# Performance work log

Hardware: AMD Instinct MI355X
Metric: run time of the kernel (lower is better)

Reference implementation:

```python
import jax, jax.numpy as jnp
import numpy as np

KUP = 5       # reassembly kernel size
DELTA = 2     # upsample ratio
KENC = 3      # encoder conv kernel size
CM = 64       # compressed channels
INC = 256
OUTC = 256


def conv2d(x, w, b, pad):
    # x: (N,C,H,W), w: (O,I,kh,kw)
    y = jax.lax.conv_general_dilated(
        x, w, window_strides=(1, 1), padding=[(pad, pad), (pad, pad)],
        dimension_numbers=("NCHW", "OIHW", "NCHW"))
    return y + b[None, :, None, None]


def pixel_shuffle(x, r):
    # torch semantics: channel c*r^2 + i*r + j -> (c, h*r+i, w*r+j)
    N, Cr2, H, W = x.shape
    C = Cr2 // (r * r)
    x = x.reshape(N, C, r, r, H, W)
    x = x.transpose(0, 1, 4, 2, 5, 3)
    return x.reshape(N, C, H * r, W * r)


def setup_inputs() -> dict:
    key = jax.random.key(0)
    ks = jax.random.split(key, 7)
    N, H, W = 4, 64, 64
    x = jax.random.normal(ks[0], (N, INC, H, W), dtype=jnp.float32)
    w_down = jax.random.normal(ks[1], (CM, INC, 1, 1), dtype=jnp.float32) * 0.05
    b_down = jnp.zeros((CM,), jnp.float32)
    enc_out = DELTA * DELTA * KUP * KUP  # 100
    w_enc = jax.random.normal(ks[2], (enc_out, CM, KENC, KENC), dtype=jnp.float32) * 0.05
    b_enc = jnp.zeros((enc_out,), jnp.float32)
    w_out = jax.random.normal(ks[3], (OUTC, INC, 1, 1), dtype=jnp.float32) * 0.05
    b_out = jnp.zeros((OUTC,), jnp.float32)
    return {"in_tensor": x, "w_down": w_down, "b_down": b_down,
            "w_enc": w_enc, "b_enc": b_enc, "w_out": w_out, "b_out": b_out}


def reference(in_tensor, w_down, b_down, w_enc, b_enc, w_out, b_out):
    N, C, H, W = in_tensor.shape
    k2, d2 = KUP * KUP, DELTA * DELTA

    # --- kernel prediction branch ---
    k = conv2d(in_tensor, w_down, b_down, 0)          # (N, Cm, H, W)
    k = conv2d(k, w_enc, b_enc, KENC // 2)            # (N, k2*d2, H, W)
    # pixel_shuffle + per-upsampled-pixel softmax over Kup^2, fused:
    # channel index = kup_idx * delta^2 + subpixel_idx (torch pixel_shuffle layout)
    k = k.reshape(N, k2, d2, H, W)
    k = jax.nn.softmax(k, axis=1)
    kern = k.transpose(0, 3, 4, 1, 2)                 # (N, H, W, k2, d2)

    # --- feature reassembly ---
    pad = KUP // 2
    xp = jnp.pad(in_tensor, ((0, 0), (0, 0), (pad, pad), (pad, pad)))
    # (N, C, H, W, Kup^2); k index = kh*Kup + kw, matching torch unfold order
    patches = jnp.stack(
        [xp[:, :, i:i + H, j:j + W] for i in range(KUP) for j in range(KUP)],
        axis=-1)

    out = jnp.einsum("nchwk,nhwkd->nhwcd", patches, kern)  # (N,H,W,C,d2)
    out = out.reshape(N, H, W, C * d2).transpose(0, 3, 1, 2)  # (N, C*d2, H, W)
    out = pixel_shuffle(out, DELTA)                   # (N, C, H*delta, W*delta)

    return conv2d(out, w_out, b_out, 0)               # (N, outC, H*delta, W*delta)
```

## Files before the change

### kernel.cpp

```cpp
#include <hip/hip_runtime.h>
#include <hip/hip_bf16.h>


namespace {
constexpr int kN = 4, kH = 64, kW = 64, kINC = 256, kCM = 64;
constexpr int kENC = 100, kH2 = 128, kW2 = 128, kOUTC = 256;
constexpr int kHW = kH * kW;
constexpr int kHW2 = kH2 * kW2;
constexpr int kPadW = 66;
constexpr int kTImg = kPadW * kPadW * kCM;
constexpr int kZPad = 68;
constexpr int kZImg = kZPad * kZPad * kOUTC;
constexpr int kPrepRepackEnc = 9 * 7 * 2 * 512;
constexpr int kPrepRepackWoz = 8 * 20 * 512;
constexpr int kPrepHaloZ = 4 * 528 * 16;
constexpr int kPrepHaloD = 4 * 260 * 8;
constexpr int kPrepTotal = kPrepRepackEnc + kPrepRepackWoz + kPrepHaloZ + kPrepHaloD;
}

typedef __attribute__((ext_vector_type(8))) short short8;
typedef __attribute__((ext_vector_type(4))) float floatx4;

static __device__ __forceinline__ unsigned short bf16bits(float f) {
  __hip_bfloat16 h = __float2bfloat16(f);
  return *(unsigned short*)&h;
}

__global__ __launch_bounds__(256) void k_prep(
    const float* __restrict__ we, unsigned short* __restrict__ Aswz,
    const float* __restrict__ wd, const float* __restrict__ wo,
    unsigned short* __restrict__ Awoz,
    float* __restrict__ zT, __hip_bfloat16* __restrict__ downT) {
  const int t = blockIdx.x * 256 + threadIdx.x;
  if (t < kPrepRepackEnc) {
    const int e = t;
    const int j = e & 7, lane = (e >> 3) & 63, kh = (e >> 9) & 1, tm = e >> 10;
    const int mt = tm % 7, tap = tm / 7;
    const int o = mt * 16 + (lane & 15);
    const int ci = kh * 32 + ((lane >> 4) & 3) * 8 + j;
    const float v = (o < kENC) ? we[(size_t)o * 576 + ci * 9 + tap] : 0.f;
    Aswz[e] = bf16bits(v);
  } else if (t < kPrepRepackEnc + kPrepRepackWoz) {
    const int e = t - kPrepRepackEnc;
    const int j = e & 7, lane = (e >> 3) & 63;
    const int rest = e >> 9;
    const int mt = rest % 20, ks = rest / 20;
    const int r = mt * 16 + (lane & 15);
    const int k = ks * 32 + (lane >> 4) * 8 + j;
    const float v = (r < kCM) ? wd[(size_t)r * kINC + k]
                              : wo[(size_t)(r - kCM) * kINC + k];
    Awoz[e] = bf16bits(v);
  } else if (t < kPrepTotal) {
    const int u0 = t - (kPrepRepackEnc + kPrepRepackWoz);
    if (u0 < kPrepHaloZ) {
      const int chunk = u0 & 15, rest = u0 >> 4;
      const int i = rest % 528, n = rest / 528;
      int r, c;
      if (i < 272) { r = i / 68; if (r >= 2) r += 64; c = i % 68; }
      else { const int j = i - 272; r = 2 + (j >> 2); const int cc = j & 3; c = (cc < 2) ? cc : cc + 64; }
      float4* p = (float4*)(zT + (size_t)n * kZImg + ((size_t)r * kZPad + c) * kOUTC) + chunk;
      *p = make_float4(0.f, 0.f, 0.f, 0.f);
    } else {
      const int u = u0 - kPrepHaloZ;
      const int chunk = u & 7, rest = u >> 3;
      const int i = rest % 260, n = rest / 260;
      int r, c;
      if (i < 132) { r = (i / 66) ? 65 : 0; c = i % 66; }
      else { const int j = i - 132; r = 1 + (j >> 1); c = (j & 1) ? 65 : 0; }
      float4* p = (float4*)((char*)downT
                  + ((size_t)n * kTImg + ((size_t)r * kPadW + c) * kCM) * 2) + chunk;
      *p = make_float4(0.f, 0.f, 0.f, 0.f);
    }
  }
}

__global__ __launch_bounds__(256) void k_dzmfma(
    const float* __restrict__ x, const unsigned short* __restrict__ Awoz,
    const float* __restrict__ bd, __hip_bfloat16* __restrict__ downT,
    float* __restrict__ zT) {
  const int b = blockIdx.x;
  const int pt = b & 255, n = b >> 8;
  const int wave = threadIdx.x >> 6, lane = threadIdx.x & 63;
  const int col = lane & 15, quad = lane >> 4;
  const int px = pt * 16 + col;
  const int h = px >> 6, w = px & 63;
  const float* xb = x + (size_t)n * kINC * kHW + px;

  floatx4 acc[5];
#pragma unroll
  for (int m = 0; m < 5; ++m) acc[m] = (floatx4){0.f, 0.f, 0.f, 0.f};

#pragma unroll
  for (int ks = 0; ks < 8; ++ks) {
    float xv[8];
#pragma unroll
    for (int j = 0; j < 8; ++j)
      xv[j] = xb[(size_t)(ks * 32 + quad * 8 + j) * kHW];
    short8 bf;
#pragma unroll
    for (int j = 0; j < 8; ++j) bf[j] = (short)bf16bits(xv[j]);
#pragma unroll
    for (int m = 0; m < 5; ++m) {
      const int wtile = wave * 5 + m;
      const short8 af = *(const short8*)(
          Awoz + ((size_t)(ks * 20 + wtile) * 64 + lane) * 8);
      acc[m] = __builtin_amdgcn_mfma_f32_16x16x32_bf16(af, bf, acc[m], 0, 0, 0);
    }
  }

#pragma unroll
  for (int m = 0; m < 5; ++m) {
    const int wtile = wave * 5 + m;
    const int r0 = wtile * 16 + quad * 4;
    if (wtile < 4) {
      union { unsigned short u[4]; uint2 v; } pk;
#pragma unroll
      for (int rr = 0; rr < 4; ++rr)
        pk.u[rr] = bf16bits(acc[m][rr] + bd[r0 + rr]);
      __hip_bfloat16* dst = downT + (size_t)n * kTImg
                            + ((h + 1) * kPadW + (w + 1)) * kCM + r0;
      *(uint2*)dst = pk.v;
    } else {
      const int o = r0 - kCM;
      float* dst = zT + (size_t)n * kZImg
                   + ((h + 2) * kZPad + (w + 2)) * kOUTC + o;
      *(float4*)dst = make_float4(acc[m][0], acc[m][1], acc[m][2], acc[m][3]);
    }
  }
}

__global__ __launch_bounds__(256) void k_encmfma(
    const __hip_bfloat16* __restrict__ downT,
    const unsigned short* __restrict__ Aswz,
    const float* __restrict__ be, float* __restrict__ enc) {
  const int b = blockIdx.x;
  const int h = b & 63, mtp = (b >> 6) & 3, n = b >> 8;
  const int wave = threadIdx.x >> 6, lane = threadIdx.x & 63;
  const int w0 = wave << 4;
  const int col = lane & 15, quad = lane >> 4;
  const int mt0 = mtp * 2;
  const bool has2 = (mt0 + 1) < 7;
  const short* dT = (const short*)downT + (size_t)n * kTImg;
  floatx4 acc0 = {0.f, 0.f, 0.f, 0.f}, acc1 = {0.f, 0.f, 0.f, 0.f};
#pragma unroll
  for (int tap = 0; tap < 9; ++tap) {
    const int dh = tap / 3 - 1, dw = tap % 3 - 1;
    const int rowbase = ((h + 1 + dh) * kPadW + (w0 + col + 1 + dw)) * kCM
                        + quad * 8;
#pragma unroll
    for (int kh = 0; kh < 2; ++kh) {
      const short8 bf = *(const short8*)(dT + rowbase + kh * 32);
      const short8 a0 = *(const short8*)(
          Aswz + (((size_t)(tap * 7 + mt0) * 2 + kh) * 64 + lane) * 8);
      acc0 = __builtin_amdgcn_mfma_f32_16x16x32_bf16(a0, bf, acc0, 0, 0, 0);
      if (has2) {
        const short8 a1 = *(const short8*)(
            Aswz + (((size_t)(tap * 7 + mt0 + 1) * 2 + kh) * 64 + lane) * 8);
        acc1 = __builtin_amdgcn_mfma_f32_16x16x32_bf16(a1, bf, acc1, 0, 0, 0);
      }
    }
  }
  const int p = h * kW + w0 + col;
#pragma unroll
  for (int r = 0; r < 4; ++r) {
    const int o = mt0 * 16 + quad * 4 + r;
    if (o < kENC) enc[(size_t)(n * kENC + o) * kHW + p] = acc0[r] + be[o];
  }
  if (has2) {
#pragma unroll
    for (int r = 0; r < 4; ++r) {
      const int o = (mt0 + 1) * 16 + quad * 4 + r;
      if (o < kENC) enc[(size_t)(n * kENC + o) * kHW + p] = acc1[r] + be[o];
    }
  }
}

__global__ __launch_bounds__(256) void k_fused_out(
    const float* __restrict__ zT, const float* __restrict__ enc,
    const float* __restrict__ bo, float* __restrict__ out) {
  const int b = blockIdx.x;
  const int pt = b & 255, og = (b >> 8) & 3, n = b >> 10;
  const int tid = threadIdx.x;
  const int wave = tid >> 6, lane = tid & 63;
  const int h = pt >> 2, w0 = (pt & 3) << 4;
  const int px0 = pt * 16;

  __shared__ float lds[64 * 65];
  float* kernLDS = lds;

  {
    const int p = tid & 15, chb = tid >> 4;
#pragma unroll
    for (int r = 0; r < 7; ++r) {
      const int ch = r * 16 + chb;
      if (ch < kENC)
        kernLDS[p * 104 + ch] = enc[((size_t)n * kENC + ch) * kHW + px0 + p];
    }
  }
  __syncthreads();

  if (tid < 64) {
    const int p = tid >> 2, d = tid & 3;
    float* kb = kernLDS + p * 104 + d;
    float m = -1e30f;
#pragma unroll
    for (int k = 0; k < 25; ++k) m = fmaxf(m, kb[k * 4]);
    float s = 0.f;
#pragma unroll
    for (int k = 0; k < 25; ++k) {
      const float e = __expf(kb[k * 4] - m);
      kb[k * 4] = e;
      s += e;
    }
    const float inv = 1.f / s;
#pragma unroll
    for (int k = 0; k < 25; ++k) kb[k * 4] *= inv;
  }
  __syncthreads();

  const int oc = lane & 15, pxi = lane >> 4;
  const int px_l = wave * 4 + pxi;
  const int w = w0 + px_l;
  const int o_l = oc * 4;
  const float* zb = zT + (size_t)n * kZImg + og * 64 + o_l;
  const float* kp = kernLDS + px_l * 104;
  float acc[4][4] = {};
#pragma unroll
  for (int tap = 0; tap < 25; ++tap) {
    const int kh = tap / 5, kw = tap % 5;
    const float4 zf = *(const float4*)(
        zb + ((size_t)(h + kh) * kZPad + (w + kw)) * kOUTC);
    const float4 kf = *(const float4*)(kp + tap * 4);
    acc[0][0] += zf.x * kf.x; acc[0][1] += zf.x * kf.y; acc[0][2] += zf.x * kf.z; acc[0][3] += zf.x * kf.w;
    acc[1][0] += zf.y * kf.x; acc[1][1] += zf.y * kf.y; acc[1][2] += zf.y * kf.z; acc[1][3] += zf.y * kf.w;
    acc[2][0] += zf.z * kf.x; acc[2][1] += zf.z * kf.y; acc[2][2] += zf.z * kf.z; acc[2][3] += zf.z * kf.w;
    acc[3][0] += zf.w * kf.x; acc[3][1] += zf.w * kf.y; acc[3][2] += zf.w * kf.z; acc[3][3] += zf.w * kf.w;
  }

  __syncthreads();
#pragma unroll
  for (int oi = 0; oi < 4; ++oi)
#pragma unroll
    for (int d = 0; d < 4; ++d)
      lds[(o_l + oi) * 65 + px_l * 4 + d] = acc[oi][d];
  __syncthreads();

  const int ol2 = tid >> 2, q = tid & 3;
  const int o = og * 64 + ol2;
  const float bias = bo[o];
  const float* Trow = lds + ol2 * 65;
#pragma unroll
  for (int i = 0; i < 2; ++i) {
    float* row = out + ((size_t)(n * kOUTC + o) * kH2 + (2 * h + i)) * kW2 + 2 * w0;
#pragma unroll
    for (int s = 0; s < 2; ++s) {
      const int xb_ = s * 16 + q * 4;
      float4 v;
      v.x = Trow[((xb_ + 0) >> 1) * 4 + i * 2 + ((xb_ + 0) & 1)] + bias;
      v.y = Trow[((xb_ + 1) >> 1) * 4 + i * 2 + ((xb_ + 1) & 1)] + bias;
      v.z = Trow[((xb_ + 2) >> 1) * 4 + i * 2 + ((xb_ + 2) & 1)] + bias;
      v.w = Trow[((xb_ + 3) >> 1) * 4 + i * 2 + ((xb_ + 3) & 1)] + bias;
      *(float4*)(row + xb_) = v;
    }
  }
}

extern "C" void kernel_launch(void* const* d_in, const int* in_sizes, int n_in,
                              void* d_out, int out_size, void* d_ws, size_t ws_size,
                              hipStream_t stream) {
  const float* x  = (const float*)d_in[0];
  const float* wd = (const float*)d_in[1];
  const float* bd = (const float*)d_in[2];
  const float* we = (const float*)d_in[3];
  const float* be = (const float*)d_in[4];
  const float* wo = (const float*)d_in[5];
  const float* bo = (const float*)d_in[6];
  float* out = (float*)d_out;

  float* enc = (float*)d_ws;
  float* zT  = enc + 1638400;
  __hip_bfloat16* downT = (__hip_bfloat16*)(zT + 4734976);
  unsigned short* Aswz  = (unsigned short*)(downT + (size_t)kN * kTImg);
  unsigned short* Awoz  = Aswz + 64512;

  k_prep<<<737, 256, 0, stream>>>(we, Aswz, wd, wo, Awoz, zT, downT);
  k_dzmfma<<<1024, 256, 0, stream>>>(x, Awoz, bd, downT, zT);
  k_encmfma<<<1024, 256, 0, stream>>>(downT, Aswz, be, enc);
  k_fused_out<<<4096, 256, 0, stream>>>(zT, enc, bo, out);
}
```

Baseline: 146.0 us.

## Fuse encoder conv into reassembly kernel, computing kernel logits per tile in LDS

Drops the separate encoder MFMA kernel and its global enc buffer. Each reassembly block now loads a 3x18x64 bf16 halo slab of the compressed features into LDS, runs the 3x3 encoder conv with MFMA for its 16 pixels, and writes the logits straight into LDS for the softmax. This removes one launch and the write and reread of the enc tensor. In exchange, the encoder conv is recomputed four times, once per output-channel group block, and each block does more work before the reassembly loop.

Result: slower. 156.7 us (+7.3%).

```diff
diff --git a/kernel.cpp b/kernel.cpp
--- a/kernel.cpp
+++ b/kernel.cpp
@@ -11,6 +11,7 @@
 constexpr int kTImg = kPadW * kPadW * kCM;
 constexpr int kZPad = 68;
 constexpr int kZImg = kZPad * kZPad * kOUTC;
+constexpr int kKP = 108;
 constexpr int kPrepRepackEnc = 9 * 7 * 2 * 512;
 constexpr int kPrepRepackWoz = 8 * 20 * 512;
 constexpr int kPrepHaloZ = 4 * 528 * 16;
@@ -129,79 +130,76 @@
   }
 }
 
-__global__ __launch_bounds__(256) void k_encmfma(
-    const __hip_bfloat16* __restrict__ downT,
-    const unsigned short* __restrict__ Aswz,
-    const float* __restrict__ be, float* __restrict__ enc) {
-  const int b = blockIdx.x;
-  const int h = b & 63, mtp = (b >> 6) & 3, n = b >> 8;
-  const int wave = threadIdx.x >> 6, lane = threadIdx.x & 63;
-  const int w0 = wave << 4;
-  const int col = lane & 15, quad = lane >> 4;
-  const int mt0 = mtp * 2;
-  const bool has2 = (mt0 + 1) < 7;
-  const short* dT = (const short*)downT + (size_t)n * kTImg;
-  floatx4 acc0 = {0.f, 0.f, 0.f, 0.f}, acc1 = {0.f, 0.f, 0.f, 0.f};
-#pragma unroll
-  for (int tap = 0; tap < 9; ++tap) {
-    const int dh = tap / 3 - 1, dw = tap % 3 - 1;
-    const int rowbase = ((h + 1 + dh) * kPadW + (w0 + col + 1 + dw)) * kCM
-                        + quad * 8;
-#pragma unroll
-    for (int kh = 0; kh < 2; ++kh) {
-      const short8 bf = *(const short8*)(dT + rowbase + kh * 32);
-      const short8 a0 = *(const short8*)(
-          Aswz + (((size_t)(tap * 7 + mt0) * 2 + kh) * 64 + lane) * 8);
-      acc0 = __builtin_amdgcn_mfma_f32_16x16x32_bf16(a0, bf, acc0, 0, 0, 0);
-      if (has2) {
-        const short8 a1 = *(const short8*)(
-            Aswz + (((size_t)(tap * 7 + mt0 + 1) * 2 + kh) * 64 + lane) * 8);
-        acc1 = __builtin_amdgcn_mfma_f32_16x16x32_bf16(a1, bf, acc1, 0, 0, 0);
-      }
-    }
-  }
-  const int p = h * kW + w0 + col;
-#pragma unroll
-  for (int r = 0; r < 4; ++r) {
-    const int o = mt0 * 16 + quad * 4 + r;
-    if (o < kENC) enc[(size_t)(n * kENC + o) * kHW + p] = acc0[r] + be[o];
-  }
-  if (has2) {
-#pragma unroll
-    for (int r = 0; r < 4; ++r) {
-      const int o = (mt0 + 1) * 16 + quad * 4 + r;
-      if (o < kENC) enc[(size_t)(n * kENC + o) * kHW + p] = acc1[r] + be[o];
-    }
-  }
-}
-
-__global__ __launch_bounds__(256) void k_fused_out(
-    const float* __restrict__ zT, const float* __restrict__ enc,
+__global__ __launch_bounds__(256) void k_tail(
+    const float* __restrict__ zT, const __hip_bfloat16* __restrict__ downT,
+    const unsigned short* __restrict__ Aswz, const float* __restrict__ be,
     const float* __restrict__ bo, float* __restrict__ out) {
   const int b = blockIdx.x;
   const int pt = b & 255, og = (b >> 8) & 3, n = b >> 10;
   const int tid = threadIdx.x;
   const int wave = tid >> 6, lane = tid & 63;
   const int h = pt >> 2, w0 = (pt & 3) << 4;
-  const int px0 = pt * 16;
-
-  __shared__ float lds[64 * 65];
+
+  __shared__ float lds[4160];
   float* kernLDS = lds;
+  unsigned short* slab = (unsigned short*)(lds + 1728);
 
   {
-    const int p = tid & 15, chb = tid >> 4;
-#pragma unroll
-    for (int r = 0; r < 7; ++r) {
-      const int ch = r * 16 + chb;
-      if (ch < kENC)
-        kernLDS[p * 104 + ch] = enc[((size_t)n * kENC + ch) * kHW + px0 + p];
+    const unsigned short* dTg = (const unsigned short*)downT + (size_t)n * kTImg;
+#pragma unroll
+    for (int it = 0; it < 2; ++it) {
+      const int idx = it * 256 + tid;
+      if (idx < 432) {
+        const int chunk = idx & 7, rowcol = idx >> 3;
+        const int row = rowcol / 18, c = rowcol % 18;
+        const short8 v = *(const short8*)(
+            dTg + (((size_t)(h + row) * kPadW) + (w0 + c)) * kCM + chunk * 8);
+        *(short8*)(slab + ((chunk * 54 + row * 18 + c) * 8)) = v;
+      }
+    }
+  }
+  __syncthreads();
+
+  {
+    const int col = lane & 15, quad = lane >> 4;
+    const int mt0 = wave * 2;
+    const bool has2 = (mt0 + 1) < 7;
+    floatx4 acc0 = {0.f, 0.f, 0.f, 0.f}, acc1 = {0.f, 0.f, 0.f, 0.f};
+#pragma unroll
+    for (int tap = 0; tap < 9; ++tap) {
+      const int dh = tap / 3, dw = tap % 3;
+#pragma unroll
+      for (int kh = 0; kh < 2; ++kh) {
+        const short8 bf = *(const short8*)(
+            slab + ((kh * 4 + quad) * 54 + dh * 18 + (col + dw)) * 8);
+        const short8 a0 = *(const short8*)(
+            Aswz + (((size_t)(tap * 7 + mt0) * 2 + kh) * 64 + lane) * 8);
+        acc0 = __builtin_amdgcn_mfma_f32_16x16x32_bf16(a0, bf, acc0, 0, 0, 0);
+        if (has2) {
+          const short8 a1 = *(const short8*)(
+              Aswz + (((size_t)(tap * 7 + mt0 + 1) * 2 + kh) * 64 + lane) * 8);
+          acc1 = __builtin_amdgcn_mfma_f32_16x16x32_bf16(a1, bf, acc1, 0, 0, 0);
+        }
+      }
+    }
+#pragma unroll
+    for (int r = 0; r < 4; ++r) {
+      const int o = mt0 * 16 + quad * 4 + r;
+      if (o < kENC) kernLDS[col * kKP + o] = acc0[r] + be[o];
+    }
+    if (has2) {
+#pragma unroll
+      for (int r = 0; r < 4; ++r) {
+        const int o = (mt0 + 1) * 16 + quad * 4 + r;
+        if (o < kENC) kernLDS[col * kKP + o] = acc1[r] + be[o];
+      }
     }
   }
   __syncthreads();
 
   if (tid < 64) {
     const int p = tid >> 2, d = tid & 3;
-    float* kb = kernLDS + p * 104 + d;
+    float* kb = kernLDS + p * kKP + d;
     float m = -1e30f;
 #pragma unroll
     for (int k = 0; k < 25; ++k) m = fmaxf(m, kb[k * 4]);
@@ -223,7 +221,7 @@
   const int w = w0 + px_l;
   const int o_l = oc * 4;
   const float* zb = zT + (size_t)n * kZImg + og * 64 + o_l;
-  const float* kp = kernLDS + px_l * 104;
+  const float* kp = kernLDS + px_l * kKP;
   float acc[4][4] = {};
 #pragma unroll
   for (int tap = 0; tap < 25; ++tap) {
@@ -285,6 +283,5 @@
 
   k_prep<<<737, 256, 0, stream>>>(we, Aswz, wd, wo, Awoz, zT, downT);
   k_dzmfma<<<1024, 256, 0, stream>>>(x, Awoz, bd, downT, zT);
-  k_encmfma<<<1024, 256, 0, stream>>>(downT, Aswz, be, enc);
-  k_fused_out<<<4096, 256, 0, stream>>>(zT, enc, bo, out);
-}
+  k_tail<<<4096, 256, 0, stream>>>(zT, downT, Aswz, be, bo, out);
+}
```
